# Kernel optimization log

Measured on AMD Instinct MI355X. Metric: run time of the kernel, lower is better.

Reference implementation:

```python
import jax, jax.numpy as jnp
import numpy as np

EMBED = 1024
HEADS = 16
HEAD_DIM = EMBED // HEADS


def setup_inputs() -> dict:
    key = jax.random.key(0)
    k1, k2, k3, k4, k5 = jax.random.split(key, 5)
    x = jax.random.normal(k1, (2, 2048, EMBED), dtype=jnp.float32)
    # torch nn.Linear params: weight [out, in], bias [out]; y = x @ W.T + b
    s_attn = 1.0 / np.sqrt(EMBED)
    w_attn = jax.random.uniform(k2, (3 * EMBED, EMBED), jnp.float32, -s_attn, s_attn)
    b_attn = jax.random.uniform(k3, (3 * EMBED,), jnp.float32, -s_attn, s_attn)
    w_proj = jax.random.uniform(k4, (EMBED, EMBED), jnp.float32, -s_attn, s_attn)
    b_proj = jax.random.uniform(k5, (EMBED,), jnp.float32, -s_attn, s_attn)
    return {"x": x, "w_attn": w_attn, "b_attn": b_attn, "w_proj": w_proj, "b_proj": b_proj}


def reference(x, w_attn, b_attn, w_proj, b_proj):
    B, S, D = x.shape
    qkv = x @ w_attn.T + b_attn                      # [B, S, 3D]
    q, k, v = jnp.split(qkv, 3, axis=-1)             # each [B, S, D]

    def heads(t):  # [B, S, D] -> [B, H, S, hd]
        return t.reshape(B, S, HEADS, HEAD_DIM).transpose(0, 2, 1, 3)

    q, k, v = heads(q), heads(k), heads(v)
    # Faithful to source: NO 1/sqrt(d) scaling, NO causal mask.
    w = jnp.einsum('bhqd,bhkd->bhqk', q, k)          # [B, H, S, S]
    w = jax.nn.softmax(w, axis=-1)
    a = jnp.einsum('bhqk,bhkd->bhqd', w, v)          # [B, H, S, hd]
    a = a.transpose(0, 2, 1, 3).reshape(B, S, D)     # merge heads
    return a @ w_proj.T + b_proj
```

## Files before the change

### kernel.cpp

```cpp
#include <hip/hip_runtime.h>
#include <hip/hip_bf16.h>
#include <stdint.h>
#include <math.h>


typedef __attribute__((ext_vector_type(2))) float f32x2;
typedef __attribute__((ext_vector_type(4))) float f32x4;
typedef __attribute__((ext_vector_type(16))) float f32x16;
typedef __attribute__((ext_vector_type(8))) short bf16x8;

static __device__ __forceinline__ unsigned short f2bf(float f) {
    unsigned u = __float_as_uint(f);
    u += 0x7FFFu + ((u >> 16) & 1u);
    return (unsigned short)(u >> 16);
}
static __device__ __forceinline__ unsigned cvt_pk_bf16(float a, float b) {
    unsigned r;
    asm("v_cvt_pk_bf16_f32 %0, %1, %2" : "=v"(r) : "v"(a), "v"(b));
    return r;
}
static __device__ __forceinline__ float fexp2(float x) {
    float r;
    asm("v_exp_f32 %0, %1" : "=v"(r) : "v"(x));
    return r;
}

typedef const __attribute__((address_space(1))) unsigned int* gas_ptr;
typedef __attribute__((address_space(3))) unsigned int* las_ptr;
static __device__ __forceinline__ void gload_lds16(const void* g, void* l) {
    __builtin_amdgcn_global_load_lds((gas_ptr)g, (las_ptr)l, 16, 0, 0);
}

__global__ void conv_all_kernel(const float* __restrict__ x,
                                const float* __restrict__ wa,
                                const float* __restrict__ wp,
                                unsigned short* __restrict__ x1,
                                unsigned short* __restrict__ w1a,
                                unsigned short* __restrict__ wpb) {
    int i = blockIdx.x * blockDim.x + threadIdx.x;
    int stride = gridDim.x * blockDim.x;
    for (; i < 2097152; i += stride) {
        const float* s; unsigned short* d; int j;
        if (i < 1048576)      { s = x;  d = x1;  j = i; }
        else if (i < 1835008) { s = wa; d = w1a; j = i - 1048576; }
        else                  { s = wp; d = wpb; j = i - 1835008; }
        float4 v = ((const float4*)s)[j];
        ushort4 o;
        o.x = f2bf(v.x); o.y = f2bf(v.y); o.z = f2bf(v.z); o.w = f2bf(v.w);
        ((ushort4*)d)[j] = o;
    }
}

__global__ __launch_bounds__(256, 2) void gemm_qkv_kernel(
    const unsigned short* __restrict__ A,
    const unsigned short* __restrict__ Bw,
    const float* __restrict__ bias,
    unsigned short* __restrict__ q1,
    unsigned short* __restrict__ k1,
    unsigned short* __restrict__ vT,
    int N, int K)
{
    __shared__ __align__(16) unsigned char lds[34816];
    const int t  = threadIdx.x;
    const int lane = t & 63;
    const int w  = t >> 6;
    const int wr = w >> 1, wc = w & 1;
    const int lg = lane >> 4, ll = lane & 15;

    const int gx = gridDim.x;
    const int flat = blockIdx.y * gx + blockIdx.x;
    const int cpx = (gx * gridDim.y) >> 3;
    const int swz = (flat & 7) * cpx + (flat >> 3);
    const int m0 = (swz / gx) * 128;
    const int n0 = (swz % gx) * 128;

    f32x4 acc[4][4] = {};

    const int srow  = t >> 3;
    const int sslot = t & 7;
    const unsigned short* Abase[4];
    const unsigned short* Bbase[4];
#pragma unroll
    for (int ci = 0; ci < 4; ++ci) {
        int r  = ci * 32 + srow;
        int cg = sslot ^ (r & 7);
        Abase[ci] = A  + (size_t)(m0 + r) * K + cg * 8;
        Bbase[ci] = Bw + (size_t)(n0 + r) * K + cg * 8;
    }

    for (int k0 = 0; k0 < K; k0 += 64) {
#pragma unroll
        for (int ci = 0; ci < 4; ++ci)
            gload_lds16(Abase[ci] + k0, lds + ci*4096 + (t>>6)*1024);
#pragma unroll
        for (int ci = 0; ci < 4; ++ci)
            gload_lds16(Bbase[ci] + k0, lds + 16384 + ci*4096 + (t>>6)*1024);
        __syncthreads();

        bf16x8 af[4][2], bfr[4][2];
#pragma unroll
        for (int mt = 0; mt < 4; ++mt)
#pragma unroll
            for (int kc = 0; kc < 2; ++kc) {
                int row = wr*64 + mt*16 + ll;
                int cg  = (4*kc + lg) ^ (row & 7);
                af[mt][kc] = *(const bf16x8*)(lds + row*128 + cg*16);
            }
#pragma unroll
        for (int nt = 0; nt < 4; ++nt)
#pragma unroll
            for (int kc = 0; kc < 2; ++kc) {
                int row = wc*64 + nt*16 + ll;
                int cg  = (4*kc + lg) ^ (row & 7);
                bfr[nt][kc] = *(const bf16x8*)(lds + 16384 + row*128 + cg*16);
            }
#pragma unroll
        for (int kc = 0; kc < 2; ++kc)
#pragma unroll
            for (int mt = 0; mt < 4; ++mt)
#pragma unroll
                for (int nt = 0; nt < 4; ++nt)
                    acc[mt][nt] = __builtin_amdgcn_mfma_f32_16x16x32_bf16(
                        af[mt][kc], bfr[nt][kc], acc[mt][nt], 0, 0, 0);
        __syncthreads();
    }

    const int TYPE = n0 >> 10;
    unsigned short* l16 = (unsigned short*)lds;
#pragma unroll
    for (int mt = 0; mt < 4; ++mt)
#pragma unroll
      for (int nt = 0; nt < 4; ++nt)
#pragma unroll
        for (int r = 0; r < 4; ++r) {
            int mp = wr*64 + mt*16 + 4*lg + r;
            int np = wc*64 + nt*16 + ll;
            float v = acc[mt][nt][r] + bias[n0 + np];
            if (TYPE == 0) v *= 1.44269504f;
            unsigned short h16 = f2bf(v);
            if (TYPE == 2) l16[np*136 + mp] = h16;
            else           l16[mp*136 + np] = h16;
        }
    __syncthreads();

    {
        const int r2 = t >> 1, half = t & 1;
        const unsigned short* src = l16 + r2*136 + half*64;
        unsigned short* dst;
        if (TYPE == 2) {
            int n = n0 + r2;
            int h = (n >> 6) & 15, d = n & 63;
            int bb = m0 >> 11;
            dst = vT + ((size_t)(bb*16 + h)*64 + d)*2048 + (m0 & 2047) + half*64;
        } else {
            int m = m0 + r2;
            int bb = m >> 11, s = m & 2047;
            int h = ((n0 + half*64) >> 6) & 15;
            dst = (TYPE == 0 ? q1 : k1) + ((size_t)(bb*16 + h)*2048 + s)*64;
        }
#pragma unroll
        for (int j = 0; j < 8; ++j)
            *(uint4*)(dst + j*8) = *(const uint4*)(src + j*8);
    }
}

__global__ __launch_bounds__(256, 2) void gemm_proj_kernel(
    const unsigned short* __restrict__ A,
    const unsigned short* __restrict__ Bw,
    const float* __restrict__ bias,
    float* __restrict__ outp)
{
    __shared__ __align__(16) unsigned char lds[24576];
    const int t  = threadIdx.x;
    const int lane = t & 63;
    const int w  = t >> 6;
    const int lg = lane >> 4, ll = lane & 15;

    const int flat = blockIdx.y * 16 + blockIdx.x;
    const int swz = (flat & 7) * 64 + (flat >> 3);
    const int m0 = (swz >> 4) * 128;
    const int n0 = (swz & 15) * 64;

    f32x4 acc[2][4] = {};

    const int srow  = t >> 3;
    const int sslot = t & 7;
    const unsigned short* Abase[4];
    const unsigned short* Bbase[2];
#pragma unroll
    for (int ci = 0; ci < 4; ++ci) {
        int r  = ci * 32 + srow;
        int cg = sslot ^ (r & 7);
        Abase[ci] = A + (size_t)(m0 + r) * 1024 + cg * 8;
    }
#pragma unroll
    for (int ci = 0; ci < 2; ++ci) {
        int r  = ci * 32 + srow;
        int cg = sslot ^ (r & 7);
        Bbase[ci] = Bw + (size_t)(n0 + r) * 1024 + cg * 8;
    }

    for (int k0 = 0; k0 < 1024; k0 += 64) {
#pragma unroll
        for (int ci = 0; ci < 4; ++ci)
            gload_lds16(Abase[ci] + k0, lds + ci*4096 + w*1024);
#pragma unroll
        for (int ci = 0; ci < 2; ++ci)
            gload_lds16(Bbase[ci] + k0, lds + 16384 + ci*4096 + w*1024);
        __syncthreads();

        bf16x8 af[2][2], bfr[4][2];
#pragma unroll
        for (int mt = 0; mt < 2; ++mt)
#pragma unroll
            for (int kc = 0; kc < 2; ++kc) {
                int row = w*32 + mt*16 + ll;
                int cg  = (4*kc + lg) ^ (row & 7);
                af[mt][kc] = *(const bf16x8*)(lds + row*128 + cg*16);
            }
#pragma unroll
        for (int nt = 0; nt < 4; ++nt)
#pragma unroll
            for (int kc = 0; kc < 2; ++kc) {
                int row = nt*16 + ll;
                int cg  = (4*kc + lg) ^ (row & 7);
                bfr[nt][kc] = *(const bf16x8*)(lds + 16384 + row*128 + cg*16);
            }
#pragma unroll
        for (int kc = 0; kc < 2; ++kc)
#pragma unroll
            for (int mt = 0; mt < 2; ++mt)
#pragma unroll
                for (int nt = 0; nt < 4; ++nt)
                    acc[mt][nt] = __builtin_amdgcn_mfma_f32_16x16x32_bf16(
                        af[mt][kc], bfr[nt][kc], acc[mt][nt], 0, 0, 0);
        __syncthreads();
    }

#pragma unroll
    for (int mt = 0; mt < 2; ++mt)
#pragma unroll
      for (int nt = 0; nt < 4; ++nt)
#pragma unroll
        for (int r = 0; r < 4; ++r) {
            int m = m0 + w*32 + mt*16 + 4*lg + r;
            int n = n0 + nt*16 + ll;
            outp[(size_t)m * 1024 + n] = acc[mt][nt][r] + bias[n];
        }
}

__global__ __launch_bounds__(512, 4) void attn_kernel(
    const unsigned short* __restrict__ q1,
    const unsigned short* __restrict__ k1,
    const unsigned short* __restrict__ vT,
    unsigned short* __restrict__ aout)
{
    __shared__ __align__(16) unsigned char lds[65536];
    const int t = threadIdx.x, lane = t & 63, w = t >> 6;
    const int hi = lane >> 5, lq = lane & 31, l7 = lane & 7;
    const int gp = w >> 2, sw = w & 3;

    const int D  = blockIdx.x;
    const int bh = (D & 7) + ((D >> 7) << 3);
    const int qb = (D >> 3) & 15;
    const int q0 = qb * 128 + sw * 32;

    bf16x8 qf[4];
    {
        const unsigned short* qp = q1 + ((size_t)bh*2048 + q0 + lq)*64 + hi*8;
#pragma unroll
        for (int ks = 0; ks < 4; ++ks)
            qf[ks] = *(const bf16x8*)(qp + ks*16);
    }

    f32x16 o0 = {}, o1 = {};
    f32x2 lr2 = {0.f, 0.f};
    const f32x16 fz = {};

    const int sr = t >> 3, ss = t & 7;
    const int scg = ss ^ (sr & 7);
    const int psr = (sr & 51) | ((sr & 4) << 1) | ((sr & 8) >> 1);
    const unsigned short* Ksrc = k1 + ((size_t)bh*2048 + psr)*64 + scg*8;
    const unsigned short* Vsrc = vT + ((size_t)bh*64 + sr)*2048 + scg*8;
    const int sdst = w*1024;

    unsigned char* fb0 = lds + gp*8192 + lq*128 + (((0 + hi) ^ l7) << 4);
    unsigned char* fb1 = lds + gp*8192 + lq*128 + (((2 + hi) ^ l7) << 4);
    unsigned char* fb2 = lds + gp*8192 + lq*128 + (((4 + hi) ^ l7) << 4);
    unsigned char* fb3 = lds + gp*8192 + lq*128 + (((6 + hi) ^ l7) << 4);

    gload_lds16(Ksrc,        lds + sdst);
    gload_lds16(Ksrc + 4096, lds + 8192 + sdst);
    gload_lds16(Vsrc,        lds + 32768 + sdst);
    gload_lds16(Vsrc + 64,   lds + 32768 + 8192 + sdst);
    __syncthreads();

#define SOFT_PACK(SV, PA, PB)                                                 \
    {                                                                         \
        float e0 =fexp2(SV[0]),  e1 =fexp2(SV[1]),  e2 =fexp2(SV[2]);         \
        float e3 =fexp2(SV[3]),  e4 =fexp2(SV[4]),  e5 =fexp2(SV[5]);         \
        float e6 =fexp2(SV[6]),  e7 =fexp2(SV[7]),  e8 =fexp2(SV[8]);         \
        float e9 =fexp2(SV[9]),  e10=fexp2(SV[10]), e11=fexp2(SV[11]);        \
        float e12=fexp2(SV[12]), e13=fexp2(SV[13]), e14=fexp2(SV[14]);        \
        float e15=fexp2(SV[15]);                                              \
        union { unsigned u[4]; bf16x8 v; } A_, B_;                            \
        A_.u[0]=cvt_pk_bf16(e0,e1);   A_.u[1]=cvt_pk_bf16(e2,e3);             \
        A_.u[2]=cvt_pk_bf16(e4,e5);   A_.u[3]=cvt_pk_bf16(e6,e7);             \
        B_.u[0]=cvt_pk_bf16(e8,e9);   B_.u[1]=cvt_pk_bf16(e10,e11);           \
        B_.u[2]=cvt_pk_bf16(e12,e13); B_.u[3]=cvt_pk_bf16(e14,e15);           \
        PA = A_.v; PB = B_.v;                                                 \
        f32x2 p0 = {e0,e1};   p0 += (f32x2){e2,e3};                           \
        p0 += (f32x2){e4,e5};   p0 += (f32x2){e6,e7};                         \
        p0 += (f32x2){e8,e9};   p0 += (f32x2){e10,e11};                       \
        p0 += (f32x2){e12,e13}; p0 += (f32x2){e14,e15};                       \
        lr2 += p0;                                                            \
    }

#define ATTN_STEP(PAR)                                                        \
    {                                                                         \
        f32x16 s0, s1;                                                        \
        bf16x8 kf;                                                            \
        __builtin_amdgcn_s_setprio(1);                                        \
                         \
        kf = *(const bf16x8*)(fb0 + (PAR)*16384);                             \
        s0 = __builtin_amdgcn_mfma_f32_32x32x16_bf16(kf, qf[0], fz, 0,0,0);   \
        kf = *(const bf16x8*)(fb1 + (PAR)*16384);                             \
        s0 = __builtin_amdgcn_mfma_f32_32x32x16_bf16(kf, qf[1], s0, 0,0,0);   \
        kf = *(const bf16x8*)(fb2 + (PAR)*16384);                             \
        s0 = __builtin_amdgcn_mfma_f32_32x32x16_bf16(kf, qf[2], s0, 0,0,0);   \
        kf = *(const bf16x8*)(fb3 + (PAR)*16384);                             \
        s0 = __builtin_amdgcn_mfma_f32_32x32x16_bf16(kf, qf[3], s0, 0,0,0);   \
        kf = *(const bf16x8*)(fb0 + (PAR)*16384 + 4096);                      \
        s1 = __builtin_amdgcn_mfma_f32_32x32x16_bf16(kf, qf[0], fz, 0,0,0);   \
        kf = *(const bf16x8*)(fb1 + (PAR)*16384 + 4096);                      \
        s1 = __builtin_amdgcn_mfma_f32_32x32x16_bf16(kf, qf[1], s1, 0,0,0);   \
        kf = *(const bf16x8*)(fb2 + (PAR)*16384 + 4096);                      \
        s1 = __builtin_amdgcn_mfma_f32_32x32x16_bf16(kf, qf[2], s1, 0,0,0);   \
        kf = *(const bf16x8*)(fb3 + (PAR)*16384 + 4096);                      \
        s1 = __builtin_amdgcn_mfma_f32_32x32x16_bf16(kf, qf[3], s1, 0,0,0);   \
        __builtin_amdgcn_s_setprio(0);                                        \
        bf16x8 pa0, pa1, pa2, pa3;                                            \
        SOFT_PACK(s0, pa0, pa1)             \
        bf16x8 vf;                                                            \
        __builtin_amdgcn_s_setprio(1);                                        \
        vf = *(const bf16x8*)(fb0 + (PAR)*16384 + 32768);                     \
        o0 = __builtin_amdgcn_mfma_f32_32x32x16_bf16(pa0, vf, o0, 0,0,0);     \
        vf = *(const bf16x8*)(fb0 + (PAR)*16384 + 32768 + 4096);              \
        o1 = __builtin_amdgcn_mfma_f32_32x32x16_bf16(pa0, vf, o1, 0,0,0);     \
        vf = *(const bf16x8*)(fb1 + (PAR)*16384 + 32768);                     \
        o0 = __builtin_amdgcn_mfma_f32_32x32x16_bf16(pa1, vf, o0, 0,0,0);     \
        vf = *(const bf16x8*)(fb1 + (PAR)*16384 + 32768 + 4096);              \
        o1 = __builtin_amdgcn_mfma_f32_32x32x16_bf16(pa1, vf, o1, 0,0,0);     \
        __builtin_amdgcn_s_setprio(0);                                        \
        SOFT_PACK(s1, pa2, pa3)      \
        __builtin_amdgcn_s_setprio(1);                                        \
        vf = *(const bf16x8*)(fb2 + (PAR)*16384 + 32768);                     \
        o0 = __builtin_amdgcn_mfma_f32_32x32x16_bf16(pa2, vf, o0, 0,0,0);     \
        vf = *(const bf16x8*)(fb2 + (PAR)*16384 + 32768 + 4096);              \
        o1 = __builtin_amdgcn_mfma_f32_32x32x16_bf16(pa2, vf, o1, 0,0,0);     \
        vf = *(const bf16x8*)(fb3 + (PAR)*16384 + 32768);                     \
        o0 = __builtin_amdgcn_mfma_f32_32x32x16_bf16(pa3, vf, o0, 0,0,0);     \
        vf = *(const bf16x8*)(fb3 + (PAR)*16384 + 32768 + 4096);              \
        o1 = __builtin_amdgcn_mfma_f32_32x32x16_bf16(pa3, vf, o1, 0,0,0);     \
        __builtin_amdgcn_s_setprio(0);                                        \
    }

    for (int sp = 0; sp < 8; ++sp) {
        {
            const size_t T = 4*(size_t)sp + 2;
            gload_lds16(Ksrc + T*4096,        lds + 16384 + sdst);
            gload_lds16(Ksrc + T*4096 + 4096, lds + 24576 + sdst);
            gload_lds16(Vsrc + T*64,          lds + 32768 + 16384 + sdst);
            gload_lds16(Vsrc + T*64 + 64,     lds + 32768 + 24576 + sdst);
            ATTN_STEP(0)
            __syncthreads();
        }
        {
            if (sp < 7) {
                const size_t T = 4*(size_t)sp + 4;
                gload_lds16(Ksrc + T*4096,        lds + sdst);
                gload_lds16(Ksrc + T*4096 + 4096, lds + 8192 + sdst);
                gload_lds16(Vsrc + T*64,          lds + 32768 + sdst);
                gload_lds16(Vsrc + T*64 + 64,     lds + 32768 + 8192 + sdst);
            }
            ATTN_STEP(1)
            __syncthreads();
        }
    }
#undef ATTN_STEP
#undef SOFT_PACK

    float lrow = lr2[0] + lr2[1];
    lrow += __shfl_xor(lrow, 32);

    float* mb = (float*)lds;
    const int slot = (sw << 6) + lane;
    if (gp == 1) {
        float* p = mb + slot * 36;
#pragma unroll
        for (int c = 0; c < 4; ++c) {
            f32x4 v = { o0[4*c], o0[4*c+1], o0[4*c+2], o0[4*c+3] };
            *(f32x4*)(p + 4*c) = v;
        }
#pragma unroll
        for (int c = 0; c < 4; ++c) {
            f32x4 v = { o1[4*c], o1[4*c+1], o1[4*c+2], o1[4*c+3] };
            *(f32x4*)(p + 16 + 4*c) = v;
        }
        p[32] = lrow;
    }
    __syncthreads();
    if (gp == 0) {
        const float* p = mb + slot * 36;
#pragma unroll
        for (int c = 0; c < 4; ++c) {
            f32x4 v = *(const f32x4*)(p + 4*c);
            o0[4*c] += v[0]; o0[4*c+1] += v[1]; o0[4*c+2] += v[2]; o0[4*c+3] += v[3];
        }
#pragma unroll
        for (int c = 0; c < 4; ++c) {
            f32x4 v = *(const f32x4*)(p + 16 + 4*c);
            o1[4*c] += v[0]; o1[4*c+1] += v[1]; o1[4*c+2] += v[2]; o1[4*c+3] += v[3];
        }
        lrow += p[32];

        const float linv_own = 1.0f / lrow;
        const int bb = bh >> 4, h = bh & 15;
#pragma unroll
        for (int r = 0; r < 16; ++r) {
            int qrow = (r & 3) + 8*(r >> 2) + 4*hi;
            float linv = __shfl(linv_own, qrow);
            size_t srow = q0 + qrow;
            aout[((size_t)(bb*2048 + srow)*16 + h)*64 + lq]      = f2bf(o0[r] * linv);
            aout[((size_t)(bb*2048 + srow)*16 + h)*64 + 32 + lq] = f2bf(o1[r] * linv);
        }
    }
}

extern "C" void kernel_launch(void* const* d_in, const int* in_sizes, int n_in,
                              void* d_out, int out_size, void* d_ws, size_t ws_size,
                              hipStream_t stream) {
    const float* x      = (const float*)d_in[0];
    const float* w_attn = (const float*)d_in[1];
    const float* b_attn = (const float*)d_in[2];
    const float* w_proj = (const float*)d_in[3];
    const float* b_proj = (const float*)d_in[4];
    float* out = (float*)d_out;

    unsigned char* ws = (unsigned char*)d_ws;
    unsigned short* x1  = (unsigned short*)(ws);
    unsigned short* w1a = (unsigned short*)(ws + (size_t)8*1024*1024);
    unsigned short* wpb = (unsigned short*)(ws + (size_t)14*1024*1024);
    unsigned short* q1  = (unsigned short*)(ws + (size_t)16*1024*1024);
    unsigned short* k1  = (unsigned short*)(ws + (size_t)24*1024*1024);
    unsigned short* vT  = (unsigned short*)(ws + (size_t)32*1024*1024);
    unsigned short* ab  = (unsigned short*)(ws + (size_t)40*1024*1024);

    conv_all_kernel<<<2048, 256, 0, stream>>>(x, w_attn, w_proj, x1, w1a, wpb);

    gemm_qkv_kernel<<<dim3(24, 32), 256, 0, stream>>>(
        x1, w1a, b_attn, q1, k1, vT, 3072, 1024);

    attn_kernel<<<512, 512, 0, stream>>>(q1, k1, vT, ab);

    gemm_proj_kernel<<<dim3(16, 32), 256, 0, stream>>>(ab, wpb, b_proj, out);
}
```

Measured before the change: 102.7 us.

## Give each attention wave two query tiles and split keys four ways

The attention kernel now has each wave hold 64 query rows (two 32-row Q fragments) instead of 32, so every K and V fragment read from LDS feeds two MFMAs. The key dimension is split across four wave groups instead of two, with smaller 32-key stages per group. The partial outputs and row sums of the four groups are then reduced through LDS in two passes. This is meant to cut LDS read traffic per MFMA. In exchange it roughly doubles accumulator registers, so launch bounds drop to 2 blocks per CU, and it adds a longer cross-group reduction at the end.

```diff
diff --git a/kernel.cpp b/kernel.cpp
--- a/kernel.cpp
+++ b/kernel.cpp
@@ -142,7 +142,6 @@
             else           l16[mp*136 + np] = h16;
         }
     __syncthreads();
-
     {
         const int r2 = t >> 1, half = t & 1;
         const unsigned short* src = l16 + r2*136 + half*64;
@@ -249,7 +248,7 @@
         }
 }
 
-__global__ __launch_bounds__(512, 4) void attn_kernel(
+__global__ __launch_bounds__(512, 2) void attn_kernel(
     const unsigned short* __restrict__ q1,
     const unsigned short* __restrict__ k1,
     const unsigned short* __restrict__ vT,
@@ -257,45 +256,59 @@
 {
     __shared__ __align__(16) unsigned char lds[65536];
     const int t = threadIdx.x, lane = t & 63, w = t >> 6;
-    const int hi = lane >> 5, lq = lane & 31, l7 = lane & 7;
-    const int gp = w >> 2, sw = w & 3;
+    const int hi = lane >> 5, lq = lane & 31;
+    const int l7 = lq & 7, l3 = lq & 3;
+    const int g = w >> 1, p = w & 1;
 
     const int D  = blockIdx.x;
     const int bh = (D & 7) + ((D >> 7) << 3);
     const int qb = (D >> 3) & 15;
-    const int q0 = qb * 128 + sw * 32;
-
-    bf16x8 qf[4];
+    const int qbase = qb * 128 + p * 64;
+
+    bf16x8 qf0[4], qf1[4];
     {
-        const unsigned short* qp = q1 + ((size_t)bh*2048 + q0 + lq)*64 + hi*8;
-#pragma unroll
-        for (int ks = 0; ks < 4; ++ks)
-            qf[ks] = *(const bf16x8*)(qp + ks*16);
-    }
-
-    f32x16 o0 = {}, o1 = {};
-    f32x2 lr2 = {0.f, 0.f};
+        const unsigned short* qp0 = q1 + ((size_t)bh*2048 + qbase + lq)*64 + hi*8;
+        const unsigned short* qp1 = qp0 + 32*64;
+#pragma unroll
+        for (int ks = 0; ks < 4; ++ks) {
+            qf0[ks] = *(const bf16x8*)(qp0 + ks*16);
+            qf1[ks] = *(const bf16x8*)(qp1 + ks*16);
+        }
+    }
+
+    f32x16 o00 = {}, o01 = {}, o10 = {}, o11 = {};
+    f32x2 lra = {0.f, 0.f}, lrb = {0.f, 0.f};
     const f32x16 fz = {};
 
-    const int sr = t >> 3, ss = t & 7;
-    const int scg = ss ^ (sr & 7);
-    const int psr = (sr & 51) | ((sr & 4) << 1) | ((sr & 8) >> 1);
-    const unsigned short* Ksrc = k1 + ((size_t)bh*2048 + psr)*64 + scg*8;
-    const unsigned short* Vsrc = vT + ((size_t)bh*64 + sr)*2048 + scg*8;
-    const int sdst = w*1024;
-
-    unsigned char* fb0 = lds + gp*8192 + lq*128 + (((0 + hi) ^ l7) << 4);
-    unsigned char* fb1 = lds + gp*8192 + lq*128 + (((2 + hi) ^ l7) << 4);
-    unsigned char* fb2 = lds + gp*8192 + lq*128 + (((4 + hi) ^ l7) << 4);
-    unsigned char* fb3 = lds + gp*8192 + lq*128 + (((6 + hi) ^ l7) << 4);
-
-    gload_lds16(Ksrc,        lds + sdst);
-    gload_lds16(Ksrc + 4096, lds + 8192 + sdst);
-    gload_lds16(Vsrc,        lds + 32768 + sdst);
-    gload_lds16(Vsrc + 64,   lds + 32768 + 8192 + sdst);
-    __syncthreads();
-
-#define SOFT_PACK(SV, PA, PB)                                                 \
+    const int sw4 = w & 3, wg = w >> 2;
+    const int rK = sw4*8 + (lane >> 3), slotK = lane & 7;
+    const int psr = (rK & ~12) | ((rK & 4) << 1) | ((rK & 8) >> 1);
+    const unsigned short* KsA = k1 + ((size_t)bh*2048 + wg*32 + psr)*64
+                                   + (slotK ^ (rK & 7))*8;
+    const unsigned short* KsB = KsA + 4096;
+    const int rV = sw4*16 + (lane >> 2), slotV = lane & 3;
+    const unsigned short* VsA = vT + ((size_t)bh*64 + rV)*2048 + wg*32
+                                   + (slotV ^ (rV & 3))*8;
+    const unsigned short* VsB = VsA + 64;
+    unsigned char* kdA = lds + wg*8192 + sw4*1024;
+    unsigned char* kdB = lds + (2+wg)*8192 + sw4*1024;
+    unsigned char* vdA = lds + 32768 + wg*8192 + sw4*1024;
+    unsigned char* vdB = lds + 32768 + (2+wg)*8192 + sw4*1024;
+
+    unsigned char* kb0 = lds + g*8192 + lq*128 + (((0+hi)^l7) << 4);
+    unsigned char* kb1 = lds + g*8192 + lq*128 + (((2+hi)^l7) << 4);
+    unsigned char* kb2 = lds + g*8192 + lq*128 + (((4+hi)^l7) << 4);
+    unsigned char* kb3 = lds + g*8192 + lq*128 + (((6+hi)^l7) << 4);
+    unsigned char* vb0 = lds + 32768 + g*8192 + lq*64 + (((0+hi)^l3) << 4);
+    unsigned char* vb1 = lds + 32768 + g*8192 + lq*64 + (((2+hi)^l3) << 4);
+
+#define STAGE(IT, PARQ)                                                       \
+    gload_lds16(KsA + (size_t)(IT)*8192, kdA + (PARQ)*4096);                  \
+    gload_lds16(KsB + (size_t)(IT)*8192, kdB + (PARQ)*4096);                  \
+    gload_lds16(VsA + (IT)*128,          vdA + (PARQ)*4096);                  \
+    gload_lds16(VsB + (IT)*128,          vdB + (PARQ)*4096);
+
+#define SOFT_PACK(SV, PA, PB, LR)                                             \
     {                                                                         \
         float e0 =fexp2(SV[0]),  e1 =fexp2(SV[1]),  e2 =fexp2(SV[2]);         \
         float e3 =fexp2(SV[3]),  e4 =fexp2(SV[4]),  e5 =fexp2(SV[5]);         \
@@ -313,126 +326,143 @@
         p0 += (f32x2){e4,e5};   p0 += (f32x2){e6,e7};                         \
         p0 += (f32x2){e8,e9};   p0 += (f32x2){e10,e11};                       \
         p0 += (f32x2){e12,e13}; p0 += (f32x2){e14,e15};                       \
-        lr2 += p0;                                                            \
-    }
-
-#define ATTN_STEP(PAR)                                                        \
+        LR += p0;                                                             \
+    }
+
+#define STEP(PARQ)                                                            \
     {                                                                         \
         f32x16 s0, s1;                                                        \
         bf16x8 kf;                                                            \
         __builtin_amdgcn_s_setprio(1);                                        \
-                         \
-        kf = *(const bf16x8*)(fb0 + (PAR)*16384);                             \
-        s0 = __builtin_amdgcn_mfma_f32_32x32x16_bf16(kf, qf[0], fz, 0,0,0);   \
-        kf = *(const bf16x8*)(fb1 + (PAR)*16384);                             \
-        s0 = __builtin_amdgcn_mfma_f32_32x32x16_bf16(kf, qf[1], s0, 0,0,0);   \
-        kf = *(const bf16x8*)(fb2 + (PAR)*16384);                             \
-        s0 = __builtin_amdgcn_mfma_f32_32x32x16_bf16(kf, qf[2], s0, 0,0,0);   \
-        kf = *(const bf16x8*)(fb3 + (PAR)*16384);                             \
-        s0 = __builtin_amdgcn_mfma_f32_32x32x16_bf16(kf, qf[3], s0, 0,0,0);   \
-        kf = *(const bf16x8*)(fb0 + (PAR)*16384 + 4096);                      \
-        s1 = __builtin_amdgcn_mfma_f32_32x32x16_bf16(kf, qf[0], fz, 0,0,0);   \
-        kf = *(const bf16x8*)(fb1 + (PAR)*16384 + 4096);                      \
-        s1 = __builtin_amdgcn_mfma_f32_32x32x16_bf16(kf, qf[1], s1, 0,0,0);   \
-        kf = *(const bf16x8*)(fb2 + (PAR)*16384 + 4096);                      \
-        s1 = __builtin_amdgcn_mfma_f32_32x32x16_bf16(kf, qf[2], s1, 0,0,0);   \
-        kf = *(const bf16x8*)(fb3 + (PAR)*16384 + 4096);                      \
-        s1 = __builtin_amdgcn_mfma_f32_32x32x16_bf16(kf, qf[3], s1, 0,0,0);   \
+        kf = *(const bf16x8*)(kb0 + (PARQ)*4096);                             \
+        s0 = __builtin_amdgcn_mfma_f32_32x32x16_bf16(kf, qf0[0], fz, 0,0,0);  \
+        s1 = __builtin_amdgcn_mfma_f32_32x32x16_bf16(kf, qf1[0], fz, 0,0,0);  \
+        kf = *(const bf16x8*)(kb1 + (PARQ)*4096);                             \
+        s0 = __builtin_amdgcn_mfma_f32_32x32x16_bf16(kf, qf0[1], s0, 0,0,0);  \
+        s1 = __builtin_amdgcn_mfma_f32_32x32x16_bf16(kf, qf1[1], s1, 0,0,0);  \
+        kf = *(const bf16x8*)(kb2 + (PARQ)*4096);                             \
+        s0 = __builtin_amdgcn_mfma_f32_32x32x16_bf16(kf, qf0[2], s0, 0,0,0);  \
+        s1 = __builtin_amdgcn_mfma_f32_32x32x16_bf16(kf, qf1[2], s1, 0,0,0);  \
+        kf = *(const bf16x8*)(kb3 + (PARQ)*4096);                             \
+        s0 = __builtin_amdgcn_mfma_f32_32x32x16_bf16(kf, qf0[3], s0, 0,0,0);  \
+        s1 = __builtin_amdgcn_mfma_f32_32x32x16_bf16(kf, qf1[3], s1, 0,0,0);  \
         __builtin_amdgcn_s_setprio(0);                                        \
-        bf16x8 pa0, pa1, pa2, pa3;                                            \
-        SOFT_PACK(s0, pa0, pa1)             \
-        bf16x8 vf;                                                            \
+        bf16x8 vf0 = *(const bf16x8*)(vb0 + (PARQ)*4096);                     \
+        bf16x8 vf1 = *(const bf16x8*)(vb0 + (PARQ)*4096 + 2048);              \
+        bf16x8 vf2 = *(const bf16x8*)(vb1 + (PARQ)*4096);                     \
+        bf16x8 vf3 = *(const bf16x8*)(vb1 + (PARQ)*4096 + 2048);              \
+        bf16x8 pa00, pa01, pa10, pa11;                                        \
+        SOFT_PACK(s0, pa00, pa01, lra)                                        \
         __builtin_amdgcn_s_setprio(1);                                        \
-        vf = *(const bf16x8*)(fb0 + (PAR)*16384 + 32768);                     \
-        o0 = __builtin_amdgcn_mfma_f32_32x32x16_bf16(pa0, vf, o0, 0,0,0);     \
-        vf = *(const bf16x8*)(fb0 + (PAR)*16384 + 32768 + 4096);              \
-        o1 = __builtin_amdgcn_mfma_f32_32x32x16_bf16(pa0, vf, o1, 0,0,0);     \
-        vf = *(const bf16x8*)(fb1 + (PAR)*16384 + 32768);                     \
-        o0 = __builtin_amdgcn_mfma_f32_32x32x16_bf16(pa1, vf, o0, 0,0,0);     \
-        vf = *(const bf16x8*)(fb1 + (PAR)*16384 + 32768 + 4096);              \
-        o1 = __builtin_amdgcn_mfma_f32_32x32x16_bf16(pa1, vf, o1, 0,0,0);     \
+        o00 = __builtin_amdgcn_mfma_f32_32x32x16_bf16(pa00, vf0, o00, 0,0,0); \
+        o01 = __builtin_amdgcn_mfma_f32_32x32x16_bf16(pa00, vf1, o01, 0,0,0); \
+        o00 = __builtin_amdgcn_mfma_f32_32x32x16_bf16(pa01, vf2, o00, 0,0,0); \
+        o01 = __builtin_amdgcn_mfma_f32_32x32x16_bf16(pa01, vf3, o01, 0,0,0); \
         __builtin_amdgcn_s_setprio(0);                                        \
-        SOFT_PACK(s1, pa2, pa3)      \
+        SOFT_PACK(s1, pa10, pa11, lrb)                                        \
         __builtin_amdgcn_s_setprio(1);                                        \
-        vf = *(const bf16x8*)(fb2 + (PAR)*16384 + 32768);                     \
-        o0 = __builtin_amdgcn_mfma_f32_32x32x16_bf16(pa2, vf, o0, 0,0,0);     \
-        vf = *(const bf16x8*)(fb2 + (PAR)*16384 + 32768 + 4096);              \
-        o1 = __builtin_amdgcn_mfma_f32_32x32x16_bf16(pa2, vf, o1, 0,0,0);     \
-        vf = *(const bf16x8*)(fb3 + (PAR)*16384 + 32768);                     \
-        o0 = __builtin_amdgcn_mfma_f32_32x32x16_bf16(pa3, vf, o0, 0,0,0);     \
-        vf = *(const bf16x8*)(fb3 + (PAR)*16384 + 32768 + 4096);              \
-        o1 = __builtin_amdgcn_mfma_f32_32x32x16_bf16(pa3, vf, o1, 0,0,0);     \
+        o10 = __builtin_amdgcn_mfma_f32_32x32x16_bf16(pa10, vf0, o10, 0,0,0); \
+        o11 = __builtin_amdgcn_mfma_f32_32x32x16_bf16(pa10, vf1, o11, 0,0,0); \
+        o10 = __builtin_amdgcn_mfma_f32_32x32x16_bf16(pa11, vf2, o10, 0,0,0); \
+        o11 = __builtin_amdgcn_mfma_f32_32x32x16_bf16(pa11, vf3, o11, 0,0,0); \
         __builtin_amdgcn_s_setprio(0);                                        \
     }
 
-    for (int sp = 0; sp < 8; ++sp) {
-        {
-            const size_t T = 4*(size_t)sp + 2;
-            gload_lds16(Ksrc + T*4096,        lds + 16384 + sdst);
-            gload_lds16(Ksrc + T*4096 + 4096, lds + 24576 + sdst);
-            gload_lds16(Vsrc + T*64,          lds + 32768 + 16384 + sdst);
-            gload_lds16(Vsrc + T*64 + 64,     lds + 32768 + 24576 + sdst);
-            ATTN_STEP(0)
-            __syncthreads();
-        }
-        {
-            if (sp < 7) {
-                const size_t T = 4*(size_t)sp + 4;
-                gload_lds16(Ksrc + T*4096,        lds + sdst);
-                gload_lds16(Ksrc + T*4096 + 4096, lds + 8192 + sdst);
-                gload_lds16(Vsrc + T*64,          lds + 32768 + sdst);
-                gload_lds16(Vsrc + T*64 + 64,     lds + 32768 + 8192 + sdst);
-            }
-            ATTN_STEP(1)
-            __syncthreads();
-        }
-    }
-#undef ATTN_STEP
+    STAGE(0, 0)
+    __syncthreads();
+
+    for (int it2 = 0; it2 < 8; ++it2) {
+        STAGE(2*it2 + 1, 1)
+        STEP(0)
+        __syncthreads();
+        if (it2 < 7) { STAGE(2*it2 + 2, 0) }
+        STEP(1)
+        __syncthreads();
+    }
+#undef STEP
 #undef SOFT_PACK
-
-    float lrow = lr2[0] + lr2[1];
-    lrow += __shfl_xor(lrow, 32);
+#undef STAGE
+
+    float la = lra[0] + lra[1];  la += __shfl_xor(la, 32);
+    float lb = lrb[0] + lrb[1];  lb += __shfl_xor(lb, 32);
 
     float* mb = (float*)lds;
-    const int slot = (sw << 6) + lane;
-    if (gp == 1) {
-        float* p = mb + slot * 36;
+    const int bb = bh >> 4, h = bh & 15;
+
+    if (g) {
+        float* pm = mb + ((((g-1)<<1) + p)*64 + lane)*36;
 #pragma unroll
         for (int c = 0; c < 4; ++c) {
-            f32x4 v = { o0[4*c], o0[4*c+1], o0[4*c+2], o0[4*c+3] };
-            *(f32x4*)(p + 4*c) = v;
-        }
-#pragma unroll
-        for (int c = 0; c < 4; ++c) {
-            f32x4 v = { o1[4*c], o1[4*c+1], o1[4*c+2], o1[4*c+3] };
-            *(f32x4*)(p + 16 + 4*c) = v;
-        }
-        p[32] = lrow;
+            f32x4 v0 = { o00[4*c], o00[4*c+1], o00[4*c+2], o00[4*c+3] };
+            *(f32x4*)(pm + 4*c) = v0;
+            f32x4 v1 = { o01[4*c], o01[4*c+1], o01[4*c+2], o01[4*c+3] };
+            *(f32x4*)(pm + 16 + 4*c) = v1;
+        }
+        pm[32] = la;
     }
     __syncthreads();
-    if (gp == 0) {
-        const float* p = mb + slot * 36;
-#pragma unroll
-        for (int c = 0; c < 4; ++c) {
-            f32x4 v = *(const f32x4*)(p + 4*c);
-            o0[4*c] += v[0]; o0[4*c+1] += v[1]; o0[4*c+2] += v[2]; o0[4*c+3] += v[3];
-        }
-#pragma unroll
-        for (int c = 0; c < 4; ++c) {
-            f32x4 v = *(const f32x4*)(p + 16 + 4*c);
-            o1[4*c] += v[0]; o1[4*c+1] += v[1]; o1[4*c+2] += v[2]; o1[4*c+3] += v[3];
-        }
-        lrow += p[32];
-
-        const float linv_own = 1.0f / lrow;
-        const int bb = bh >> 4, h = bh & 15;
+    if (g == 0) {
+#pragma unroll
+        for (int s = 0; s < 3; ++s) {
+            const float* pm = mb + (((s<<1) + p)*64 + lane)*36;
+#pragma unroll
+            for (int c = 0; c < 4; ++c) {
+                f32x4 v0 = *(const f32x4*)(pm + 4*c);
+                o00[4*c] += v0[0]; o00[4*c+1] += v0[1];
+                o00[4*c+2] += v0[2]; o00[4*c+3] += v0[3];
+                f32x4 v1 = *(const f32x4*)(pm + 16 + 4*c);
+                o01[4*c] += v1[0]; o01[4*c+1] += v1[1];
+                o01[4*c+2] += v1[2]; o01[4*c+3] += v1[3];
+            }
+            la += pm[32];
+        }
+        const float linv_own = 1.0f / la;
 #pragma unroll
         for (int r = 0; r < 16; ++r) {
             int qrow = (r & 3) + 8*(r >> 2) + 4*hi;
             float linv = __shfl(linv_own, qrow);
-            size_t srow = q0 + qrow;
-            aout[((size_t)(bb*2048 + srow)*16 + h)*64 + lq]      = f2bf(o0[r] * linv);
-            aout[((size_t)(bb*2048 + srow)*16 + h)*64 + 32 + lq] = f2bf(o1[r] * linv);
+            size_t srow = qbase + qrow;
+            aout[((size_t)(bb*2048 + srow)*16 + h)*64 + lq]      = f2bf(o00[r] * linv);
+            aout[((size_t)(bb*2048 + srow)*16 + h)*64 + 32 + lq] = f2bf(o01[r] * linv);
+        }
+    }
+    __syncthreads();
+
+    if (g) {
+        float* pm = mb + ((((g-1)<<1) + p)*64 + lane)*36;
+#pragma unroll
+        for (int c = 0; c < 4; ++c) {
+            f32x4 v0 = { o10[4*c], o10[4*c+1], o10[4*c+2], o10[4*c+3] };
+            *(f32x4*)(pm + 4*c) = v0;
+            f32x4 v1 = { o11[4*c], o11[4*c+1], o11[4*c+2], o11[4*c+3] };
+            *(f32x4*)(pm + 16 + 4*c) = v1;
+        }
+        pm[32] = lb;
+    }
+    __syncthreads();
+    if (g == 0) {
+#pragma unroll
+        for (int s = 0; s < 3; ++s) {
+            const float* pm = mb + (((s<<1) + p)*64 + lane)*36;
+#pragma unroll
+            for (int c = 0; c < 4; ++c) {
+                f32x4 v0 = *(const f32x4*)(pm + 4*c);
+                o10[4*c] += v0[0]; o10[4*c+1] += v0[1];
+                o10[4*c+2] += v0[2]; o10[4*c+3] += v0[3];
+                f32x4 v1 = *(const f32x4*)(pm + 16 + 4*c);
+                o11[4*c] += v1[0]; o11[4*c+1] += v1[1];
+                o11[4*c+2] += v1[2]; o11[4*c+3] += v1[3];
+            }
+            lb += pm[32];
+        }
+        const float linv_own = 1.0f / lb;
+#pragma unroll
+        for (int r = 0; r < 16; ++r) {
+            int qrow = (r & 3) + 8*(r >> 2) + 4*hi;
+            float linv = __shfl(linv_own, qrow);
+            size_t srow = qbase + 32 + qrow;
+            aout[((size_t)(bb*2048 + srow)*16 + h)*64 + lq]      = f2bf(o10[r] * linv);
+            aout[((size_t)(bb*2048 + srow)*16 + h)*64 + 32 + lq] = f2bf(o11[r] * linv);
         }
     }
 }
```

After: 107.1 us. +4.3%, slower.

## Process two 32-row query tiles per wave to reuse K/V fragments

Applied to the files above, without the earlier changes.

Each attention wave now handles 64 query rows (two Q fragment sets), so every K and V fragment read from LDS feeds two MFMAs. The block count halves to 256 and the launch bound drops to 2 blocks per CU to make room for the doubled accumulators. This cuts LDS traffic and global K/V reloads per query. The cost is higher register pressure and fewer blocks, which leaves only one wave of blocks on 256 CUs and less latency hiding.

```diff
diff --git a/kernel.cpp b/kernel.cpp
--- a/kernel.cpp
+++ b/kernel.cpp
@@ -142,7 +142,6 @@
             else           l16[mp*136 + np] = h16;
         }
     __syncthreads();
-
     {
         const int r2 = t >> 1, half = t & 1;
         const unsigned short* src = l16 + r2*136 + half*64;
@@ -249,7 +248,7 @@
         }
 }
 
-__global__ __launch_bounds__(512, 4) void attn_kernel(
+__global__ __launch_bounds__(512, 2) void attn_kernel(
     const unsigned short* __restrict__ q1,
     const unsigned short* __restrict__ k1,
     const unsigned short* __restrict__ vT,
@@ -261,20 +260,23 @@
     const int gp = w >> 2, sw = w & 3;
 
     const int D  = blockIdx.x;
-    const int bh = (D & 7) + ((D >> 7) << 3);
-    const int qb = (D >> 3) & 15;
-    const int q0 = qb * 128 + sw * 32;
-
-    bf16x8 qf[4];
+    const int bh = (D & 7) + ((D >> 6) << 3);
+    const int qb = (D >> 3) & 7;
+    const int q0 = qb * 256 + sw * 64;
+
+    bf16x8 qfA[4], qfB[4];
     {
-        const unsigned short* qp = q1 + ((size_t)bh*2048 + q0 + lq)*64 + hi*8;
-#pragma unroll
-        for (int ks = 0; ks < 4; ++ks)
-            qf[ks] = *(const bf16x8*)(qp + ks*16);
-    }
-
-    f32x16 o0 = {}, o1 = {};
-    f32x2 lr2 = {0.f, 0.f};
+        const unsigned short* qpA = q1 + ((size_t)bh*2048 + q0 + lq)*64 + hi*8;
+        const unsigned short* qpB = qpA + 32*64;
+#pragma unroll
+        for (int ks = 0; ks < 4; ++ks) {
+            qfA[ks] = *(const bf16x8*)(qpA + ks*16);
+            qfB[ks] = *(const bf16x8*)(qpB + ks*16);
+        }
+    }
+
+    f32x16 oA0 = {}, oA1 = {}, oB0 = {}, oB1 = {};
+    f32x2 lra = {0.f, 0.f}, lrb = {0.f, 0.f};
     const f32x16 fz = {};
 
     const int sr = t >> 3, ss = t & 7;
@@ -295,7 +297,7 @@
     gload_lds16(Vsrc + 64,   lds + 32768 + 8192 + sdst);
     __syncthreads();
 
-#define SOFT_PACK(SV, PA, PB)                                                 \
+#define SOFT_PACK(SV, PA, PB, LR)                                             \
     {                                                                         \
         float e0 =fexp2(SV[0]),  e1 =fexp2(SV[1]),  e2 =fexp2(SV[2]);         \
         float e3 =fexp2(SV[3]),  e4 =fexp2(SV[4]),  e5 =fexp2(SV[5]);         \
@@ -313,55 +315,80 @@
         p0 += (f32x2){e4,e5};   p0 += (f32x2){e6,e7};                         \
         p0 += (f32x2){e8,e9};   p0 += (f32x2){e10,e11};                       \
         p0 += (f32x2){e12,e13}; p0 += (f32x2){e14,e15};                       \
-        lr2 += p0;                                                            \
-    }
-
-#define ATTN_STEP(PAR)                                                        \
+        LR += p0;                                                             \
+    }
+
+#define STEP(PAR)                                                             \
     {                                                                         \
-        f32x16 s0, s1;                                                        \
+        f32x16 sA0, sA1, sB0, sB1;                                            \
         bf16x8 kf;                                                            \
         __builtin_amdgcn_s_setprio(1);                                        \
-                         \
         kf = *(const bf16x8*)(fb0 + (PAR)*16384);                             \
-        s0 = __builtin_amdgcn_mfma_f32_32x32x16_bf16(kf, qf[0], fz, 0,0,0);   \
+        sA0 = __builtin_amdgcn_mfma_f32_32x32x16_bf16(kf, qfA[0], fz, 0,0,0); \
+        sB0 = __builtin_amdgcn_mfma_f32_32x32x16_bf16(kf, qfB[0], fz, 0,0,0); \
+        kf = *(const bf16x8*)(fb0 + (PAR)*16384 + 4096);                      \
+        sA1 = __builtin_amdgcn_mfma_f32_32x32x16_bf16(kf, qfA[0], fz, 0,0,0); \
+        sB1 = __builtin_amdgcn_mfma_f32_32x32x16_bf16(kf, qfB[0], fz, 0,0,0); \
         kf = *(const bf16x8*)(fb1 + (PAR)*16384);                             \
-        s0 = __builtin_amdgcn_mfma_f32_32x32x16_bf16(kf, qf[1], s0, 0,0,0);   \
+        sA0 = __builtin_amdgcn_mfma_f32_32x32x16_bf16(kf, qfA[1], sA0, 0,0,0);\
+        sB0 = __builtin_amdgcn_mfma_f32_32x32x16_bf16(kf, qfB[1], sB0, 0,0,0);\
+        kf = *(const bf16x8*)(fb1 + (PAR)*16384 + 4096);                      \
+        sA1 = __builtin_amdgcn_mfma_f32_32x32x16_bf16(kf, qfA[1], sA1, 0,0,0);\
+        sB1 = __builtin_amdgcn_mfma_f32_32x32x16_bf16(kf, qfB[1], sB1, 0,0,0);\
         kf = *(const bf16x8*)(fb2 + (PAR)*16384);                             \
-        s0 = __builtin_amdgcn_mfma_f32_32x32x16_bf16(kf, qf[2], s0, 0,0,0);   \
+        sA0 = __builtin_amdgcn_mfma_f32_32x32x16_bf16(kf, qfA[2], sA0, 0,0,0);\
+        sB0 = __builtin_amdgcn_mfma_f32_32x32x16_bf16(kf, qfB[2], sB0, 0,0,0);\
+        kf = *(const bf16x8*)(fb2 + (PAR)*16384 + 4096);                      \
+        sA1 = __builtin_amdgcn_mfma_f32_32x32x16_bf16(kf, qfA[2], sA1, 0,0,0);\
+        sB1 = __builtin_amdgcn_mfma_f32_32x32x16_bf16(kf, qfB[2], sB1, 0,0,0);\
         kf = *(const bf16x8*)(fb3 + (PAR)*16384);                             \
-        s0 = __builtin_amdgcn_mfma_f32_32x32x16_bf16(kf, qf[3], s0, 0,0,0);   \
-        kf = *(const bf16x8*)(fb0 + (PAR)*16384 + 4096);                      \
-        s1 = __builtin_amdgcn_mfma_f32_32x32x16_bf16(kf, qf[0], fz, 0,0,0);   \
-        kf = *(const bf16x8*)(fb1 + (PAR)*16384 + 4096);                      \
-        s1 = __builtin_amdgcn_mfma_f32_32x32x16_bf16(kf, qf[1], s1, 0,0,0);   \
-        kf = *(const bf16x8*)(fb2 + (PAR)*16384 + 4096);                      \
-        s1 = __builtin_amdgcn_mfma_f32_32x32x16_bf16(kf, qf[2], s1, 0,0,0);   \
+        sA0 = __builtin_amdgcn_mfma_f32_32x32x16_bf16(kf, qfA[3], sA0, 0,0,0);\
+        sB0 = __builtin_amdgcn_mfma_f32_32x32x16_bf16(kf, qfB[3], sB0, 0,0,0);\
         kf = *(const bf16x8*)(fb3 + (PAR)*16384 + 4096);                      \
-        s1 = __builtin_amdgcn_mfma_f32_32x32x16_bf16(kf, qf[3], s1, 0,0,0);   \
+        sA1 = __builtin_amdgcn_mfma_f32_32x32x16_bf16(kf, qfA[3], sA1, 0,0,0);\
+        sB1 = __builtin_amdgcn_mfma_f32_32x32x16_bf16(kf, qfB[3], sB1, 0,0,0);\
         __builtin_amdgcn_s_setprio(0);                                        \
         bf16x8 pa0, pa1, pa2, pa3;                                            \
-        SOFT_PACK(s0, pa0, pa1)             \
         bf16x8 vf;                                                            \
+        SOFT_PACK(sA0, pa0, pa1, lra)                                         \
+        SOFT_PACK(sA1, pa2, pa3, lra)                                         \
         __builtin_amdgcn_s_setprio(1);                                        \
         vf = *(const bf16x8*)(fb0 + (PAR)*16384 + 32768);                     \
-        o0 = __builtin_amdgcn_mfma_f32_32x32x16_bf16(pa0, vf, o0, 0,0,0);     \
+        oA0 = __builtin_amdgcn_mfma_f32_32x32x16_bf16(pa0, vf, oA0, 0,0,0);   \
         vf = *(const bf16x8*)(fb0 + (PAR)*16384 + 32768 + 4096);              \
-        o1 = __builtin_amdgcn_mfma_f32_32x32x16_bf16(pa0, vf, o1, 0,0,0);     \
+        oA1 = __builtin_amdgcn_mfma_f32_32x32x16_bf16(pa0, vf, oA1, 0,0,0);   \
         vf = *(const bf16x8*)(fb1 + (PAR)*16384 + 32768);                     \
-        o0 = __builtin_amdgcn_mfma_f32_32x32x16_bf16(pa1, vf, o0, 0,0,0);     \
+        oA0 = __builtin_amdgcn_mfma_f32_32x32x16_bf16(pa1, vf, oA0, 0,0,0);   \
         vf = *(const bf16x8*)(fb1 + (PAR)*16384 + 32768 + 4096);              \
-        o1 = __builtin_amdgcn_mfma_f32_32x32x16_bf16(pa1, vf, o1, 0,0,0);     \
+        oA1 = __builtin_amdgcn_mfma_f32_32x32x16_bf16(pa1, vf, oA1, 0,0,0);   \
+        vf = *(const bf16x8*)(fb2 + (PAR)*16384 + 32768);                     \
+        oA0 = __builtin_amdgcn_mfma_f32_32x32x16_bf16(pa2, vf, oA0, 0,0,0);   \
+        vf = *(const bf16x8*)(fb2 + (PAR)*16384 + 32768 + 4096);              \
+        oA1 = __builtin_amdgcn_mfma_f32_32x32x16_bf16(pa2, vf, oA1, 0,0,0);   \
+        vf = *(const bf16x8*)(fb3 + (PAR)*16384 + 32768);                     \
+        oA0 = __builtin_amdgcn_mfma_f32_32x32x16_bf16(pa3, vf, oA0, 0,0,0);   \
+        vf = *(const bf16x8*)(fb3 + (PAR)*16384 + 32768 + 4096);              \
+        oA1 = __builtin_amdgcn_mfma_f32_32x32x16_bf16(pa3, vf, oA1, 0,0,0);   \
         __builtin_amdgcn_s_setprio(0);                                        \
-        SOFT_PACK(s1, pa2, pa3)      \
+        SOFT_PACK(sB0, pa0, pa1, lrb)                                         \
+        SOFT_PACK(sB1, pa2, pa3, lrb)                                         \
         __builtin_amdgcn_s_setprio(1);                                        \
+        vf = *(const bf16x8*)(fb0 + (PAR)*16384 + 32768);                     \
+        oB0 = __builtin_amdgcn_mfma_f32_32x32x16_bf16(pa0, vf, oB0, 0,0,0);   \
+        vf = *(const bf16x8*)(fb0 + (PAR)*16384 + 32768 + 4096);              \
+        oB1 = __builtin_amdgcn_mfma_f32_32x32x16_bf16(pa0, vf, oB1, 0,0,0);   \
+        vf = *(const bf16x8*)(fb1 + (PAR)*16384 + 32768);                     \
+        oB0 = __builtin_amdgcn_mfma_f32_32x32x16_bf16(pa1, vf, oB0, 0,0,0);   \
+        vf = *(const bf16x8*)(fb1 + (PAR)*16384 + 32768 + 4096);              \
+        oB1 = __builtin_amdgcn_mfma_f32_32x32x16_bf16(pa1, vf, oB1, 0,0,0);   \
         vf = *(const bf16x8*)(fb2 + (PAR)*16384 + 32768);                     \
-        o0 = __builtin_amdgcn_mfma_f32_32x32x16_bf16(pa2, vf, o0, 0,0,0);     \
+        oB0 = __builtin_amdgcn_mfma_f32_32x32x16_bf16(pa2, vf, oB0, 0,0,0);   \
         vf = *(const bf16x8*)(fb2 + (PAR)*16384 + 32768 + 4096);              \
-        o1 = __builtin_amdgcn_mfma_f32_32x32x16_bf16(pa2, vf, o1, 0,0,0);     \
+        oB1 = __builtin_amdgcn_mfma_f32_32x32x16_bf16(pa2, vf, oB1, 0,0,0);   \
         vf = *(const bf16x8*)(fb3 + (PAR)*16384 + 32768);                     \
-        o0 = __builtin_amdgcn_mfma_f32_32x32x16_bf16(pa3, vf, o0, 0,0,0);     \
+        oB0 = __builtin_amdgcn_mfma_f32_32x32x16_bf16(pa3, vf, oB0, 0,0,0);   \
         vf = *(const bf16x8*)(fb3 + (PAR)*16384 + 32768 + 4096);              \
-        o1 = __builtin_amdgcn_mfma_f32_32x32x16_bf16(pa3, vf, o1, 0,0,0);     \
+        oB1 = __builtin_amdgcn_mfma_f32_32x32x16_bf16(pa3, vf, oB1, 0,0,0);   \
         __builtin_amdgcn_s_setprio(0);                                        \
     }
 
@@ -372,7 +399,7 @@
             gload_lds16(Ksrc + T*4096 + 4096, lds + 24576 + sdst);
             gload_lds16(Vsrc + T*64,          lds + 32768 + 16384 + sdst);
             gload_lds16(Vsrc + T*64 + 64,     lds + 32768 + 24576 + sdst);
-            ATTN_STEP(0)
+            STEP(0)
             __syncthreads();
         }
         {
@@ -383,56 +410,88 @@
                 gload_lds16(Vsrc + T*64,          lds + 32768 + sdst);
                 gload_lds16(Vsrc + T*64 + 64,     lds + 32768 + 8192 + sdst);
             }
-            ATTN_STEP(1)
+            STEP(1)
             __syncthreads();
         }
     }
-#undef ATTN_STEP
+#undef STEP
 #undef SOFT_PACK
 
-    float lrow = lr2[0] + lr2[1];
-    lrow += __shfl_xor(lrow, 32);
+    float la = lra[0] + lra[1];  la += __shfl_xor(la, 32);
+    float lb = lrb[0] + lrb[1];  lb += __shfl_xor(lb, 32);
 
     float* mb = (float*)lds;
     const int slot = (sw << 6) + lane;
+    const int bb = bh >> 4, h = bh & 15;
+
     if (gp == 1) {
         float* p = mb + slot * 36;
 #pragma unroll
         for (int c = 0; c < 4; ++c) {
-            f32x4 v = { o0[4*c], o0[4*c+1], o0[4*c+2], o0[4*c+3] };
-            *(f32x4*)(p + 4*c) = v;
-        }
-#pragma unroll
-        for (int c = 0; c < 4; ++c) {
-            f32x4 v = { o1[4*c], o1[4*c+1], o1[4*c+2], o1[4*c+3] };
-            *(f32x4*)(p + 16 + 4*c) = v;
-        }
-        p[32] = lrow;
+            f32x4 v0 = { oA0[4*c], oA0[4*c+1], oA0[4*c+2], oA0[4*c+3] };
+            *(f32x4*)(p + 4*c) = v0;
+            f32x4 v1 = { oA1[4*c], oA1[4*c+1], oA1[4*c+2], oA1[4*c+3] };
+            *(f32x4*)(p + 16 + 4*c) = v1;
+        }
+        p[32] = la;
     }
     __syncthreads();
     if (gp == 0) {
         const float* p = mb + slot * 36;
 #pragma unroll
         for (int c = 0; c < 4; ++c) {
-            f32x4 v = *(const f32x4*)(p + 4*c);
-            o0[4*c] += v[0]; o0[4*c+1] += v[1]; o0[4*c+2] += v[2]; o0[4*c+3] += v[3];
-        }
-#pragma unroll
-        for (int c = 0; c < 4; ++c) {
-            f32x4 v = *(const f32x4*)(p + 16 + 4*c);
-            o1[4*c] += v[0]; o1[4*c+1] += v[1]; o1[4*c+2] += v[2]; o1[4*c+3] += v[3];
-        }
-        lrow += p[32];
-
-        const float linv_own = 1.0f / lrow;
-        const int bb = bh >> 4, h = bh & 15;
+            f32x4 v0 = *(const f32x4*)(p + 4*c);
+            oA0[4*c] += v0[0]; oA0[4*c+1] += v0[1];
+            oA0[4*c+2] += v0[2]; oA0[4*c+3] += v0[3];
+            f32x4 v1 = *(const f32x4*)(p + 16 + 4*c);
+            oA1[4*c] += v1[0]; oA1[4*c+1] += v1[1];
+            oA1[4*c+2] += v1[2]; oA1[4*c+3] += v1[3];
+        }
+        la += p[32];
+        const float linv_own = 1.0f / la;
 #pragma unroll
         for (int r = 0; r < 16; ++r) {
             int qrow = (r & 3) + 8*(r >> 2) + 4*hi;
             float linv = __shfl(linv_own, qrow);
             size_t srow = q0 + qrow;
-            aout[((size_t)(bb*2048 + srow)*16 + h)*64 + lq]      = f2bf(o0[r] * linv);
-            aout[((size_t)(bb*2048 + srow)*16 + h)*64 + 32 + lq] = f2bf(o1[r] * linv);
+            aout[((size_t)(bb*2048 + srow)*16 + h)*64 + lq]      = f2bf(oA0[r] * linv);
+            aout[((size_t)(bb*2048 + srow)*16 + h)*64 + 32 + lq] = f2bf(oA1[r] * linv);
+        }
+    }
+    __syncthreads();
+
+    if (gp == 1) {
+        float* p = mb + slot * 36;
+#pragma unroll
+        for (int c = 0; c < 4; ++c) {
+            f32x4 v0 = { oB0[4*c], oB0[4*c+1], oB0[4*c+2], oB0[4*c+3] };
+            *(f32x4*)(p + 4*c) = v0;
+            f32x4 v1 = { oB1[4*c], oB1[4*c+1], oB1[4*c+2], oB1[4*c+3] };
+            *(f32x4*)(p + 16 + 4*c) = v1;
+        }
+        p[32] = lb;
+    }
+    __syncthreads();
+    if (gp == 0) {
+        const float* p = mb + slot * 36;
+#pragma unroll
+        for (int c = 0; c < 4; ++c) {
+            f32x4 v0 = *(const f32x4*)(p + 4*c);
+            oB0[4*c] += v0[0]; oB0[4*c+1] += v0[1];
+            oB0[4*c+2] += v0[2]; oB0[4*c+3] += v0[3];
+            f32x4 v1 = *(const f32x4*)(p + 16 + 4*c);
+            oB1[4*c] += v1[0]; oB1[4*c+1] += v1[1];
+            oB1[4*c+2] += v1[2]; oB1[4*c+3] += v1[3];
+        }
+        lb += p[32];
+        const float linv_own = 1.0f / lb;
+#pragma unroll
+        for (int r = 0; r < 16; ++r) {
+            int qrow = (r & 3) + 8*(r >> 2) + 4*hi;
+            float linv = __shfl(linv_own, qrow);
+            size_t srow = q0 + 32 + qrow;
+            aout[((size_t)(bb*2048 + srow)*16 + h)*64 + lq]      = f2bf(oB0[r] * linv);
+            aout[((size_t)(bb*2048 + srow)*16 + h)*64 + 32 + lq] = f2bf(oB1[r] * linv);
         }
     }
 }
@@ -461,7 +520,7 @@
     gemm_qkv_kernel<<<dim3(24, 32), 256, 0, stream>>>(
         x1, w1a, b_attn, q1, k1, vT, 3072, 1024);
 
-    attn_kernel<<<512, 512, 0, stream>>>(q1, k1, vT, ab);
+    attn_kernel<<<256, 512, 0, stream>>>(q1, k1, vT, ab);
 
     gemm_proj_kernel<<<dim3(16, 32), 256, 0, stream>>>(ab, wpb, b_proj, out);
 }
```

Measured after the change: 102.5 us. Within noise of the previous version (-0.3%).
